# Performance work log

Hardware: AMD Instinct MI355X
Metric: run time of the kernel (lower is better)

## Reference

```python
import jax, jax.numpy as jnp
import numpy as np

N_NODES = 20000
N_EDGES = 640000
IN_DIM = 256
HID = 128
N_GRAPHS = 64


def setup_inputs() -> dict:
    key = jax.random.key(0)
    ks = jax.random.split(key, 9)
    x = jax.random.normal(ks[0], (N_NODES, IN_DIM), jnp.float32)
    edge_index = jax.random.randint(ks[1], (2, N_EDGES), 0, N_NODES, dtype=jnp.int32)
    batch = jnp.sort(jax.random.randint(ks[2], (N_NODES,), 0, N_GRAPHS, dtype=jnp.int32))

    def lin(k, fan_in, fan_out):
        # torch.nn.Linear default init: U(-1/sqrt(fan_in), 1/sqrt(fan_in))
        bound = 1.0 / np.sqrt(fan_in)
        kw, kb = jax.random.split(k)
        W = jax.random.uniform(kw, (fan_in, fan_out), jnp.float32, -bound, bound)
        b = jax.random.uniform(kb, (fan_out,), jnp.float32, -bound, bound)
        return W, b

    W0, b0 = lin(ks[3], IN_DIM, HID)
    W1, b1 = lin(ks[4], HID, HID)
    W2, b2 = lin(ks[5], HID, HID)
    return dict(x=x, edge_index=edge_index, batch=batch,
                W0=W0, b0=b0, W1=W1, b1=b1, W2=W2, b2=b2)


def reference(x, edge_index, batch, W0, b0, W1, b1, W2, b2):
    src, dst = edge_index[0], edge_index[1]
    edge_batch = batch[src]  # [E] segment id per edge
    ones = jnp.ones((edge_batch.shape[0], 1), x.dtype)
    counts = jax.ops.segment_sum(ones, edge_batch, num_segments=N_GRAPHS)
    inv_counts = 1.0 / jnp.maximum(counts, 1.0)

    def pool(z):
        # gather endpoint features, concat -> [E, 2*HID], mean pool by graph
        edge_emb = jnp.concatenate([z[src], z[dst]], axis=1)
        return jax.ops.segment_sum(edge_emb, edge_batch, num_segments=N_GRAPHS) * inv_counts

    g = []
    z = x
    for W, b in ((W0, b0), (W1, b1), (W2, b2)):
        z = z @ W + b
        g.append(pool(z))
    return jnp.concatenate(g, axis=1)  # [N_GRAPHS, 3 * 2 * HID]
```

## Files before the change

kernel.cpp:

```cpp
#include <hip/hip_runtime.h>

#define N_NODES 20000
#define N_EDGES 640000
#define N_GRAPHS 64

#define NCHUNK 128
#define CHUNK_SZ 157
#define GSPLIT 8
#define GSUB 8

#define GCAP 12288
#define BG_TILE 2048
#define NBG 313

#define CD_OFF      0
#define DEG_OFF     1280000
#define CNT_OFF     1300000
#define CUR_OFF     1300064
#define Y_OFF       1300128
#define PART_OFF    1332896
#define PAIRS_OFF   3430048

__global__ __launch_bounds__(256) void bucket_g_k(const int* __restrict__ ei,
                                                  const int* __restrict__ batch,
                                                  unsigned long long* __restrict__ pairs,
                                                  unsigned* __restrict__ cursor,
                                                  float* __restrict__ Y,
                                                  float* __restrict__ deg) {
    __shared__ unsigned hist[N_GRAPHS];
    __shared__ unsigned gbase[N_GRAPHS];
    const int t = threadIdx.x;
    if (t < N_GRAPHS) hist[t] = 0u;
    __syncthreads();

    const int e0 = blockIdx.x * BG_TILE;
    int sv[8], dv[8];
    unsigned rnk[8], gg[8];
#pragma unroll
    for (int k = 0; k < 8; ++k) {
        int e = e0 + t + k * 256;
        if (e < N_EDGES) {
            int s = ei[e];
            int d = ei[N_EDGES + e];
            int g = batch[s];
            sv[k] = s; dv[k] = d; gg[k] = (unsigned)g;
            rnk[k] = atomicAdd(&hist[g], 1u);
        } else {
            gg[k] = 0xFFFFFFFFu;
        }
    }
    __syncthreads();
    if (t < N_GRAPHS) {
        unsigned c = hist[t];
        gbase[t] = c ? atomicAdd(&cursor[t], c) : 0u;
    }
    __syncthreads();
#pragma unroll
    for (int k = 0; k < 8; ++k) {
        unsigned g = gg[k];
        if (g != 0xFFFFFFFFu) {
            unsigned slot = gbase[g] + rnk[k];
            if (slot < GCAP)
                pairs[(size_t)g * GCAP + slot] =
                    ((unsigned long long)(unsigned)sv[k] << 32) | (unsigned)dv[k];
        }
    }
    if (blockIdx.x == 0) {
        float4* y4 = (float4*)Y;
        for (int i = t; i < 64 * 64; i += 256) y4[i] = make_float4(0.f, 0.f, 0.f, 0.f);
        float4* d4 = (float4*)deg;
        for (int i = t; i < N_NODES / 4; i += 256) d4[i] = make_float4(0.f, 0.f, 0.f, 0.f);
    }
}

__global__ __launch_bounds__(1024) void cd_col_k(const unsigned long long* __restrict__ pairs,
                                                 const unsigned* __restrict__ cursor,
                                                 float* __restrict__ Cdcol,
                                                 float* __restrict__ deg,
                                                 float* __restrict__ counts) {
    __shared__ unsigned dh[N_NODES / 2];
    __shared__ unsigned sh2[N_NODES / 2];
    const int t = threadIdx.x;
    const int g = blockIdx.x;
    for (int i = t; i < N_NODES / 2; i += 1024) { dh[i] = 0u; sh2[i] = 0u; }
    __syncthreads();

    unsigned cnt = cursor[g];
    if (cnt > GCAP) cnt = GCAP;
    const unsigned long long* pv = pairs + (size_t)g * GCAP;
    for (unsigned i = t; i < cnt; i += 1024) {
        unsigned long long p = pv[i];
        unsigned s = (unsigned)(p >> 32);
        unsigned d = (unsigned)p;
        atomicAdd(&dh[d >> 1], 1u << ((d & 1u) * 16));
        atomicAdd(&sh2[s >> 1], 1u << ((s & 1u) * 16));
    }
    __syncthreads();

    float2* outc = (float2*)(Cdcol + (size_t)g * N_NODES);
    for (int w = t; w < N_NODES / 2; w += 1024) {
        unsigned v = dh[w];
        outc[w] = make_float2((float)(v & 0xFFFFu), (float)(v >> 16));
        unsigned u = sh2[w];
        if (u & 0xFFFFu) deg[2 * w]     = (float)(u & 0xFFFFu);
        if (u >> 16)     deg[2 * w + 1] = (float)(u >> 16);
    }
    if (t == 0) counts[g] = (float)cnt;
}

#define FMA8(C0, C1, XV)                                          \
    acc[0].x = fmaf(C0.x, XV.x, acc[0].x); acc[0].y = fmaf(C0.x, XV.y, acc[0].y); \
    acc[0].z = fmaf(C0.x, XV.z, acc[0].z); acc[0].w = fmaf(C0.x, XV.w, acc[0].w); \
    acc[1].x = fmaf(C0.y, XV.x, acc[1].x); acc[1].y = fmaf(C0.y, XV.y, acc[1].y); \
    acc[1].z = fmaf(C0.y, XV.z, acc[1].z); acc[1].w = fmaf(C0.y, XV.w, acc[1].w); \
    acc[2].x = fmaf(C0.z, XV.x, acc[2].x); acc[2].y = fmaf(C0.z, XV.y, acc[2].y); \
    acc[2].z = fmaf(C0.z, XV.z, acc[2].z); acc[2].w = fmaf(C0.z, XV.w, acc[2].w); \
    acc[3].x = fmaf(C0.w, XV.x, acc[3].x); acc[3].y = fmaf(C0.w, XV.y, acc[3].y); \
    acc[3].z = fmaf(C0.w, XV.z, acc[3].z); acc[3].w = fmaf(C0.w, XV.w, acc[3].w); \
    acc[4].x = fmaf(C1.x, XV.x, acc[4].x); acc[4].y = fmaf(C1.x, XV.y, acc[4].y); \
    acc[4].z = fmaf(C1.x, XV.z, acc[4].z); acc[4].w = fmaf(C1.x, XV.w, acc[4].w); \
    acc[5].x = fmaf(C1.y, XV.x, acc[5].x); acc[5].y = fmaf(C1.y, XV.y, acc[5].y); \
    acc[5].z = fmaf(C1.y, XV.z, acc[5].z); acc[5].w = fmaf(C1.y, XV.w, acc[5].w); \
    acc[6].x = fmaf(C1.z, XV.x, acc[6].x); acc[6].y = fmaf(C1.z, XV.y, acc[6].y); \
    acc[6].z = fmaf(C1.z, XV.z, acc[6].z); acc[6].w = fmaf(C1.z, XV.w, acc[6].w); \
    acc[7].x = fmaf(C1.w, XV.x, acc[7].x); acc[7].y = fmaf(C1.w, XV.y, acc[7].y); \
    acc[7].z = fmaf(C1.w, XV.z, acc[7].z); acc[7].w = fmaf(C1.w, XV.w, acc[7].w);

__global__ __launch_bounds__(256) void pool_k(const float* __restrict__ x,
                                              const int* __restrict__ batch,
                                              const float* __restrict__ Cdcol,
                                              const float* __restrict__ deg,
                                              float* __restrict__ Y,
                                              float* __restrict__ part) {
    __shared__ float4 sc4[CHUNK_SZ * 2];
    __shared__ float sdeg[CHUNK_SZ];
    __shared__ int   sbatch[CHUNK_SZ];
    __shared__ float4 red[2 * GSUB * 64];

    const int t = threadIdx.x;
    const int fg = t & 63;
    const int p  = t >> 6;
    const int b = blockIdx.x & 127;
    const int j = blockIdx.x >> 7;
    const int n0 = b * CHUNK_SZ;
    const int cnt = (n0 + CHUNK_SZ <= N_NODES) ? CHUNK_SZ : (N_NODES - n0);

    float* sc = (float*)sc4;
    const float* cbase = Cdcol + (size_t)(j * GSUB) * N_NODES + n0;
#pragma unroll
    for (int k = 0; k < GSUB; ++k)
        for (int i = t; i < cnt; i += 256)
            sc[i * GSUB + k] = cbase[(size_t)k * N_NODES + i];
    if (j == 0) {
        for (int i = t; i < cnt; i += 256) {
            sdeg[i] = deg[n0 + i];
            sbatch[i] = batch[n0 + i];
        }
    }
    __syncthreads();

    const float4* x4 = (const float4*)x;
    float4 acc[GSUB];
#pragma unroll
    for (int k = 0; k < GSUB; ++k) acc[k] = make_float4(0.f, 0.f, 0.f, 0.f);

    if (j == 0) {
        float4 accs = make_float4(0.f, 0.f, 0.f, 0.f);
        int gprev = (p < cnt) ? sbatch[p] : 0;
        int i = p;
        float4 xn = make_float4(0.f, 0.f, 0.f, 0.f);
        if (i < cnt) xn = x4[(size_t)(n0 + i) * 64 + fg];
        for (; i < cnt; i += 4) {
            float4 xv = xn;
            if (i + 4 < cnt) xn = x4[(size_t)(n0 + i + 4) * 64 + fg];
            int g = sbatch[i];
            if (g != gprev) {
                float* yr = Y + gprev * 256 + fg * 4;
                atomicAdd(yr + 0, accs.x); atomicAdd(yr + 1, accs.y);
                atomicAdd(yr + 2, accs.z); atomicAdd(yr + 3, accs.w);
                accs = make_float4(0.f, 0.f, 0.f, 0.f);
                gprev = g;
            }
            float dg = sdeg[i];
            accs.x = fmaf(dg, xv.x, accs.x); accs.y = fmaf(dg, xv.y, accs.y);
            accs.z = fmaf(dg, xv.z, accs.z); accs.w = fmaf(dg, xv.w, accs.w);
            float4 c0 = sc4[i * 2], c1 = sc4[i * 2 + 1];
            FMA8(c0, c1, xv)
        }
        if (p < cnt) {
            float* yr = Y + gprev * 256 + fg * 4;
            atomicAdd(yr + 0, accs.x); atomicAdd(yr + 1, accs.y);
            atomicAdd(yr + 2, accs.z); atomicAdd(yr + 3, accs.w);
        }
    } else {
        int i = p;
        float4 xn = make_float4(0.f, 0.f, 0.f, 0.f);
        if (i < cnt) xn = x4[(size_t)(n0 + i) * 64 + fg];
        for (; i < cnt; i += 4) {
            float4 xv = xn;
            if (i + 4 < cnt) xn = x4[(size_t)(n0 + i + 4) * 64 + fg];
            float4 c0 = sc4[i * 2], c1 = sc4[i * 2 + 1];
            FMA8(c0, c1, xv)
        }
    }

    if (p >= 2) {
#pragma unroll
        for (int k = 0; k < GSUB; ++k) red[(p - 2) * (GSUB * 64) + k * 64 + fg] = acc[k];
    }
    __syncthreads();
    if (p < 2) {
#pragma unroll
        for (int k = 0; k < GSUB; ++k) {
            float4 v = red[p * (GSUB * 64) + k * 64 + fg];
            acc[k].x += v.x; acc[k].y += v.y; acc[k].z += v.z; acc[k].w += v.w;
        }
    }
    __syncthreads();
    if (p == 1) {
#pragma unroll
        for (int k = 0; k < GSUB; ++k) red[k * 64 + fg] = acc[k];
    }
    __syncthreads();
    if (p == 0) {
        float4* part4 = (float4*)part;
#pragma unroll
        for (int k = 0; k < GSUB; ++k) {
            float4 v = red[k * 64 + fg];
            acc[k].x += v.x; acc[k].y += v.y; acc[k].z += v.z; acc[k].w += v.w;
            part4[(size_t)(b * 64 + j * GSUB + k) * 64 + fg] = acc[k];
        }
    }
}

__global__ __launch_bounds__(256) void reduce_k(const float* __restrict__ part,
                                                float* __restrict__ Y) {
    __shared__ float4 red[3 * 64];
    const int j = blockIdx.x;
    const int l = threadIdx.x & 63;
    const int h = threadIdx.x >> 6;
    const float4* part4 = (const float4*)part;
    float4 s = make_float4(0.f, 0.f, 0.f, 0.f);
    for (int bb = h * 32; bb < h * 32 + 32; ++bb) {
        float4 v = part4[(size_t)(bb * 64 + j) * 64 + l];
        s.x += v.x; s.y += v.y; s.z += v.z; s.w += v.w;
    }
    if (h > 0) red[(h - 1) * 64 + l] = s;
    __syncthreads();
    if (h == 0) {
#pragma unroll
        for (int q = 0; q < 3; ++q) {
            float4 v = red[q * 64 + l];
            s.x += v.x; s.y += v.y; s.z += v.z; s.w += v.w;
        }
        ((float4*)(Y + (64 + j) * 256))[l] = s;
    }
}

__global__ __launch_bounds__(128) void chain_k(const float* __restrict__ Y,
                                               const float* __restrict__ counts,
                                               const float* __restrict__ W0, const float* __restrict__ b0,
                                               const float* __restrict__ W1, const float* __restrict__ b1,
                                               const float* __restrict__ W2, const float* __restrict__ b2,
                                               float* __restrict__ out) {
    __shared__ float m[256];
    __shared__ float h[128];
    const int r = blockIdx.x;
    const int f = threadIdx.x;
    const int g = r & 63;
    const int half = (r >= 64) ? 128 : 0;

    float c = counts[g];
    float inv = 1.0f / fmaxf(c, 1.0f);
    float beta = c * inv;

    m[f]       = Y[r * 256 + f]       * inv;
    m[f + 128] = Y[r * 256 + f + 128] * inv;
    __syncthreads();

    float s1 = 0.0f;
    for (int k = 0; k < 256; ++k) s1 += m[k] * W0[k * 128 + f];
    s1 += beta * b0[f];
    out[g * 768 + 0 + half + f] = s1;
    h[f] = s1;
    __syncthreads();

    float s2 = 0.0f;
    for (int k = 0; k < 128; ++k) s2 += h[k] * W1[k * 128 + f];
    s2 += beta * b1[f];
    out[g * 768 + 256 + half + f] = s2;
    __syncthreads();
    h[f] = s2;
    __syncthreads();

    float s3 = 0.0f;
    for (int k = 0; k < 128; ++k) s3 += h[k] * W2[k * 128 + f];
    s3 += beta * b2[f];
    out[g * 768 + 512 + half + f] = s3;
}

extern "C" void kernel_launch(void* const* d_in, const int* in_sizes, int n_in,
                              void* d_out, int out_size, void* d_ws, size_t ws_size,
                              hipStream_t stream) {
    const float* x     = (const float*)d_in[0];
    const int*   ei    = (const int*)d_in[1];
    const int*   batch = (const int*)d_in[2];
    const float* W0    = (const float*)d_in[3];
    const float* b0    = (const float*)d_in[4];
    const float* W1    = (const float*)d_in[5];
    const float* b1    = (const float*)d_in[6];
    const float* W2    = (const float*)d_in[7];
    const float* b2    = (const float*)d_in[8];
    float* out = (float*)d_out;

    float*    ws     = (float*)d_ws;
    float*    Cdcol  = ws + CD_OFF;
    float*    deg    = ws + DEG_OFF;
    float*    counts = ws + CNT_OFF;
    unsigned* cursor = (unsigned*)(ws + CUR_OFF);
    float*    Y      = ws + Y_OFF;
    float*    part   = ws + PART_OFF;
    unsigned long long* pairs = (unsigned long long*)(ws + PAIRS_OFF);

    hipMemsetAsync(cursor, 0, N_GRAPHS * sizeof(unsigned), stream);
    bucket_g_k<<<NBG, 256, 0, stream>>>(ei, batch, pairs, cursor, Y, deg);
    cd_col_k<<<N_GRAPHS, 1024, 0, stream>>>(pairs, cursor, Cdcol, deg, counts);
    pool_k<<<NCHUNK * GSPLIT, 256, 0, stream>>>(x, batch, Cdcol, deg, Y, part);
    reduce_k<<<64, 256, 0, stream>>>(part, Y);
    chain_k<<<128, 128, 0, stream>>>(Y, counts, W0, b0, W1, b1, W2, b2, out);
}
```

Measured before the change: 140.2 us.

## Replace global-cursor edge bucketing with per-block segments and fuse reduce into chain

Edge bucketing now writes packed 32-bit (src<<15|dst) values into fixed per-(graph,block) segments with a per-block histogram, instead of using global atomic cursors and 64-bit pairs. This removes the memset and the cross-block atomics. The degree/column kernel is split four ways per graph over destination ranges, and source degrees are computed only within each graph's node range, found by binary search on the sorted batch array. The separate reduce kernel is folded into the chain kernel, which removes one launch. In exchange, any per-block bucket above SEGCAP edges is silently truncated, and the cd pass scans padded slots.

Result: slower. 163.3 us (+16.5%).

```diff
diff --git a/kernel.cpp b/kernel.cpp
--- a/kernel.cpp
+++ b/kernel.cpp
@@ -9,103 +9,127 @@
 #define GSPLIT 8
 #define GSUB 8
 
-#define GCAP 12288
 #define BG_TILE 2048
 #define NBG 313
+#define SEGCAP 80
+#define GR_CAP 768
 
 #define CD_OFF      0
 #define DEG_OFF     1280000
 #define CNT_OFF     1300000
-#define CUR_OFF     1300064
-#define Y_OFF       1300128
-#define PART_OFF    1332896
-#define PAIRS_OFF   3430048
+#define Y_OFF       1300064
+#define PART_OFF    1316448
+#define BH_OFF      3413600
+#define VALS_OFF    3433632
 
 __global__ __launch_bounds__(256) void bucket_g_k(const int* __restrict__ ei,
                                                   const int* __restrict__ batch,
-                                                  unsigned long long* __restrict__ pairs,
-                                                  unsigned* __restrict__ cursor,
-                                                  float* __restrict__ Y,
-                                                  float* __restrict__ deg) {
+                                                  unsigned* __restrict__ vals,
+                                                  unsigned* __restrict__ bh,
+                                                  float* __restrict__ Y) {
     __shared__ unsigned hist[N_GRAPHS];
-    __shared__ unsigned gbase[N_GRAPHS];
     const int t = threadIdx.x;
+    const int blk = blockIdx.x;
     if (t < N_GRAPHS) hist[t] = 0u;
     __syncthreads();
 
-    const int e0 = blockIdx.x * BG_TILE;
-    int sv[8], dv[8];
-    unsigned rnk[8], gg[8];
+    const int e0 = blk * BG_TILE;
+    unsigned pv[8], rnk[8], gg[8];
 #pragma unroll
     for (int k = 0; k < 8; ++k) {
         int e = e0 + t + k * 256;
         if (e < N_EDGES) {
-            int s = ei[e];
-            int d = ei[N_EDGES + e];
-            int g = batch[s];
-            sv[k] = s; dv[k] = d; gg[k] = (unsigned)g;
+            unsigned s = (unsigned)ei[e];
+            unsigned d = (unsigned)ei[N_EDGES + e];
+            unsigned g = (unsigned)batch[s];
+            pv[k] = (s << 15) | d;
+            gg[k] = g;
             rnk[k] = atomicAdd(&hist[g], 1u);
         } else {
             gg[k] = 0xFFFFFFFFu;
         }
     }
+#pragma unroll
+    for (int k = 0; k < 8; ++k) {
+        unsigned g = gg[k];
+        if (g != 0xFFFFFFFFu && rnk[k] < SEGCAP)
+            vals[((size_t)g * NBG + blk) * SEGCAP + rnk[k]] = pv[k];
+    }
     __syncthreads();
     if (t < N_GRAPHS) {
         unsigned c = hist[t];
-        gbase[t] = c ? atomicAdd(&cursor[t], c) : 0u;
-    }
-    __syncthreads();
-#pragma unroll
-    for (int k = 0; k < 8; ++k) {
-        unsigned g = gg[k];
-        if (g != 0xFFFFFFFFu) {
-            unsigned slot = gbase[g] + rnk[k];
-            if (slot < GCAP)
-                pairs[(size_t)g * GCAP + slot] =
-                    ((unsigned long long)(unsigned)sv[k] << 32) | (unsigned)dv[k];
-        }
-    }
-    if (blockIdx.x == 0) {
+        bh[blk * N_GRAPHS + t] = (c > SEGCAP) ? SEGCAP : c;
+    }
+    if (blk == 0) {
         float4* y4 = (float4*)Y;
         for (int i = t; i < 64 * 64; i += 256) y4[i] = make_float4(0.f, 0.f, 0.f, 0.f);
-        float4* d4 = (float4*)deg;
-        for (int i = t; i < N_NODES / 4; i += 256) d4[i] = make_float4(0.f, 0.f, 0.f, 0.f);
-    }
-}
-
-__global__ __launch_bounds__(1024) void cd_col_k(const unsigned long long* __restrict__ pairs,
-                                                 const unsigned* __restrict__ cursor,
-                                                 float* __restrict__ Cdcol,
-                                                 float* __restrict__ deg,
-                                                 float* __restrict__ counts) {
-    __shared__ unsigned dh[N_NODES / 2];
-    __shared__ unsigned sh2[N_NODES / 2];
+    }
+}
+
+__global__ __launch_bounds__(256) void cd_col_k(const unsigned* __restrict__ vals,
+                                                const unsigned* __restrict__ bh,
+                                                const int* __restrict__ batch,
+                                                float* __restrict__ Cdcol,
+                                                float* __restrict__ deg,
+                                                float* __restrict__ counts) {
+    __shared__ unsigned scnt[NBG];
+    __shared__ unsigned dh[2500];
+    __shared__ unsigned sdeg[GR_CAP];
+    __shared__ int s_lo, s_hi;
+    __shared__ unsigned s_tot;
     const int t = threadIdx.x;
-    const int g = blockIdx.x;
-    for (int i = t; i < N_NODES / 2; i += 1024) { dh[i] = 0u; sh2[i] = 0u; }
-    __syncthreads();
-
-    unsigned cnt = cursor[g];
-    if (cnt > GCAP) cnt = GCAP;
-    const unsigned long long* pv = pairs + (size_t)g * GCAP;
-    for (unsigned i = t; i < cnt; i += 1024) {
-        unsigned long long p = pv[i];
-        unsigned s = (unsigned)(p >> 32);
-        unsigned d = (unsigned)p;
-        atomicAdd(&dh[d >> 1], 1u << ((d & 1u) * 16));
-        atomicAdd(&sh2[s >> 1], 1u << ((s & 1u) * 16));
-    }
-    __syncthreads();
-
-    float2* outc = (float2*)(Cdcol + (size_t)g * N_NODES);
-    for (int w = t; w < N_NODES / 2; w += 1024) {
+    const int g = blockIdx.x >> 2;
+    const int q = blockIdx.x & 3;
+    const int d0 = q * 5000;
+
+    for (int i = t; i < NBG; i += 256) scnt[i] = bh[i * N_GRAPHS + g];
+    for (int i = t; i < 2500; i += 256) dh[i] = 0u;
+    if (q == 0) {
+        for (int i = t; i < GR_CAP; i += 256) sdeg[i] = 0u;
+        if (t == 0) {
+            int lo = 0, hi = N_NODES;
+            while (lo < hi) { int m = (lo + hi) >> 1; if (batch[m] < g) lo = m + 1; else hi = m; }
+            s_lo = lo;
+            int lo2 = lo; hi = N_NODES;
+            while (lo2 < hi) { int m = (lo2 + hi) >> 1; if (batch[m] < g + 1) lo2 = m + 1; else hi = m; }
+            s_hi = lo2;
+        }
+    }
+    __syncthreads();
+    const int lo = s_lo;
+
+    const unsigned* vg = vals + (size_t)g * NBG * SEGCAP;
+    for (int idx = t; idx < NBG * SEGCAP; idx += 256) {
+        unsigned blk = (unsigned)idx / SEGCAP;
+        unsigned slot = (unsigned)idx - blk * SEGCAP;
+        if (slot < scnt[blk]) {
+            unsigned v = vg[idx];
+            int d = (int)(v & 0x7FFFu);
+            int rd = d - d0;
+            if ((unsigned)rd < 5000u)
+                atomicAdd(&dh[rd >> 1], 1u << ((rd & 1) * 16));
+            if (q == 0) {
+                int rs = (int)(v >> 15) - lo;
+                if ((unsigned)rs < (unsigned)GR_CAP) atomicAdd(&sdeg[rs], 1u);
+            }
+        }
+    }
+    __syncthreads();
+
+    float2* outc = (float2*)(Cdcol + (size_t)g * N_NODES + d0);
+    for (int w = t; w < 2500; w += 256) {
         unsigned v = dh[w];
         outc[w] = make_float2((float)(v & 0xFFFFu), (float)(v >> 16));
-        unsigned u = sh2[w];
-        if (u & 0xFFFFu) deg[2 * w]     = (float)(u & 0xFFFFu);
-        if (u >> 16)     deg[2 * w + 1] = (float)(u >> 16);
-    }
-    if (t == 0) counts[g] = (float)cnt;
+    }
+    if (q == 0) {
+        const int range = s_hi - lo;
+        for (int i = t; i < range; i += 256) deg[lo + i] = (float)sdeg[i];
+        if (t == 0) {
+            unsigned tot = 0;
+            for (int i = 0; i < NBG; ++i) tot += scnt[i];
+            counts[g] = (float)tot;
+        }
+    }
 }
 
 #define FMA8(C0, C1, XV)                                          \
@@ -233,40 +257,17 @@
     }
 }
 
-__global__ __launch_bounds__(256) void reduce_k(const float* __restrict__ part,
-                                                float* __restrict__ Y) {
-    __shared__ float4 red[3 * 64];
-    const int j = blockIdx.x;
-    const int l = threadIdx.x & 63;
-    const int h = threadIdx.x >> 6;
-    const float4* part4 = (const float4*)part;
-    float4 s = make_float4(0.f, 0.f, 0.f, 0.f);
-    for (int bb = h * 32; bb < h * 32 + 32; ++bb) {
-        float4 v = part4[(size_t)(bb * 64 + j) * 64 + l];
-        s.x += v.x; s.y += v.y; s.z += v.z; s.w += v.w;
-    }
-    if (h > 0) red[(h - 1) * 64 + l] = s;
-    __syncthreads();
-    if (h == 0) {
-#pragma unroll
-        for (int q = 0; q < 3; ++q) {
-            float4 v = red[q * 64 + l];
-            s.x += v.x; s.y += v.y; s.z += v.z; s.w += v.w;
-        }
-        ((float4*)(Y + (64 + j) * 256))[l] = s;
-    }
-}
-
-__global__ __launch_bounds__(128) void chain_k(const float* __restrict__ Y,
-                                               const float* __restrict__ counts,
-                                               const float* __restrict__ W0, const float* __restrict__ b0,
-                                               const float* __restrict__ W1, const float* __restrict__ b1,
-                                               const float* __restrict__ W2, const float* __restrict__ b2,
-                                               float* __restrict__ out) {
+__global__ __launch_bounds__(256) void chain2_k(const float* __restrict__ Y,
+                                                const float* __restrict__ part,
+                                                const float* __restrict__ counts,
+                                                const float* __restrict__ W0, const float* __restrict__ b0,
+                                                const float* __restrict__ W1, const float* __restrict__ b1,
+                                                const float* __restrict__ W2, const float* __restrict__ b2,
+                                                float* __restrict__ out) {
     __shared__ float m[256];
     __shared__ float h[128];
     const int r = blockIdx.x;
-    const int f = threadIdx.x;
+    const int t = threadIdx.x;
     const int g = r & 63;
     const int half = (r >= 64) ? 128 : 0;
 
@@ -274,29 +275,38 @@
     float inv = 1.0f / fmaxf(c, 1.0f);
     float beta = c * inv;
 
-    m[f]       = Y[r * 256 + f]       * inv;
-    m[f + 128] = Y[r * 256 + f + 128] * inv;
-    __syncthreads();
-
-    float s1 = 0.0f;
-    for (int k = 0; k < 256; ++k) s1 += m[k] * W0[k * 128 + f];
-    s1 += beta * b0[f];
-    out[g * 768 + 0 + half + f] = s1;
-    h[f] = s1;
-    __syncthreads();
-
+    if (r < 64) {
+        m[t] = Y[r * 256 + t] * inv;
+    } else {
+        float s = 0.0f;
+        for (int bb = 0; bb < NCHUNK; ++bb) s += part[(size_t)(bb * 64 + g) * 256 + t];
+        m[t] = s * inv;
+    }
+    __syncthreads();
+
+    if (t < 128) {
+        float s1 = 0.0f;
+        for (int k = 0; k < 256; ++k) s1 += m[k] * W0[k * 128 + t];
+        s1 += beta * b0[t];
+        out[g * 768 + 0 + half + t] = s1;
+        h[t] = s1;
+    }
+    __syncthreads();
     float s2 = 0.0f;
-    for (int k = 0; k < 128; ++k) s2 += h[k] * W1[k * 128 + f];
-    s2 += beta * b1[f];
-    out[g * 768 + 256 + half + f] = s2;
-    __syncthreads();
-    h[f] = s2;
-    __syncthreads();
-
-    float s3 = 0.0f;
-    for (int k = 0; k < 128; ++k) s3 += h[k] * W2[k * 128 + f];
-    s3 += beta * b2[f];
-    out[g * 768 + 512 + half + f] = s3;
+    if (t < 128) {
+        for (int k = 0; k < 128; ++k) s2 += h[k] * W1[k * 128 + t];
+        s2 += beta * b1[t];
+        out[g * 768 + 256 + half + t] = s2;
+    }
+    __syncthreads();
+    if (t < 128) h[t] = s2;
+    __syncthreads();
+    if (t < 128) {
+        float s3 = 0.0f;
+        for (int k = 0; k < 128; ++k) s3 += h[k] * W2[k * 128 + t];
+        s3 += beta * b2[t];
+        out[g * 768 + 512 + half + t] = s3;
+    }
 }
 
 extern "C" void kernel_launch(void* const* d_in, const int* in_sizes, int n_in,
@@ -317,15 +327,13 @@
     float*    Cdcol  = ws + CD_OFF;
     float*    deg    = ws + DEG_OFF;
     float*    counts = ws + CNT_OFF;
-    unsigned* cursor = (unsigned*)(ws + CUR_OFF);
     float*    Y      = ws + Y_OFF;
     float*    part   = ws + PART_OFF;
-    unsigned long long* pairs = (unsigned long long*)(ws + PAIRS_OFF);
-
-    hipMemsetAsync(cursor, 0, N_GRAPHS * sizeof(unsigned), stream);
-    bucket_g_k<<<NBG, 256, 0, stream>>>(ei, batch, pairs, cursor, Y, deg);
-    cd_col_k<<<N_GRAPHS, 1024, 0, stream>>>(pairs, cursor, Cdcol, deg, counts);
+    unsigned* bh     = (unsigned*)(ws + BH_OFF);
+    unsigned* vals   = (unsigned*)(ws + VALS_OFF);
+
+    bucket_g_k<<<NBG, 256, 0, stream>>>(ei, batch, vals, bh, Y);
+    cd_col_k<<<N_GRAPHS * 4, 256, 0, stream>>>(vals, bh, batch, Cdcol, deg, counts);
     pool_k<<<NCHUNK * GSPLIT, 256, 0, stream>>>(x, batch, Cdcol, deg, Y, part);
-    reduce_k<<<64, 256, 0, stream>>>(part, Y);
-    chain_k<<<128, 128, 0, stream>>>(Y, counts, W0, b0, W1, b1, W2, b2, out);
-}
+    chain2_k<<<128, 256, 0, stream>>>(Y, part, counts, W0, b0, W1, b1, W2, b2, out);
+}
```
